# Optimization experiments

Measured on AMD Instinct MI355X. Metric: run time of the kernel, lower is better.

Reference implementation:

```python
import jax, jax.numpy as jnp
import numpy as np

TAU = 20.0   # membrane time constant (init default)
TH = 1.0     # spike threshold (init default)
K = 10.0     # surrogate sigmoid slope (hard-coded in forward)
EPS = 1e-6


def setup_inputs() -> dict:
    key = jax.random.key(0)
    I = jax.random.normal(key, (4096, 4096), dtype=jnp.float32)  # [B, L]
    return {"I": I}


def reference(I):
    B, L = I.shape

    def step(v, I_t):
        # Euler: dv = -v/tau + I ; v <- v + dv
        v = v - v / TAU + I_t
        s_soft = jax.nn.sigmoid(K * (v - TH))
        s_hard = (v >= TH).astype(I.dtype)
        # straight-through: value = s_hard, gradient flows through s_soft
        s = jax.lax.stop_gradient(s_hard - s_soft) + s_soft
        # reset: v <- v * (1 - stopgrad(s)); stopgrad(s) has value s_hard
        v = v * (1.0 - s_hard)
        return v, (s, s_hard)

    v0 = jnp.zeros((B,), dtype=I.dtype)
    _, (spikes_t, hard_t) = jax.lax.scan(step, v0, I.T)  # xs: [L, B]
    spikes = spikes_t.T       # [B, L]
    hard_spikes = hard_t.T    # [B, L]

    # hard latency: index of first hard spike, else L
    fired = hard_spikes > 0.5
    has = jnp.any(fired, axis=1)
    idx = jnp.argmax(fired, axis=1)
    hard_latency = jnp.where(has, idx, L).astype(jnp.int32)  # [B]

    # soft latency: spike-weighted mean time
    time = jnp.arange(L, dtype=spikes.dtype)
    w = spikes / (spikes.sum(axis=1, keepdims=True) + EPS)
    soft_latency = (w * time).sum(axis=1)  # [B]

    return spikes, hard_latency, soft_latency
```

## Files before the change

kernel.cpp:

```cpp
#include <hip/hip_runtime.h>

#define B_DIM 4096
#define L_DIM 4096
#define SEGLEN 512
#define NSEG (L_DIM / SEGLEN)
#define WARM 512
#define CHUNK 64
#define LSTRIDE 68

typedef float f4 __attribute__((ext_vector_type(4)));

__global__ __launch_bounds__(256) void init_kernel(float* wsf, int* wsi) {
    int i = blockIdx.x * 256 + threadIdx.x;
    if (i < 2 * B_DIM) wsf[i] = 0.f;
    if (i < B_DIM) wsi[i] = L_DIM;
}

#define LIF_CORE(IIN)                         \
    float q0 = u * cdiv;                      \
    float rr = fmaf(-20.0f, q0, u);           \
    float q  = fmaf(rr, cdiv, q0);            \
    float a  = u - q;                         \
    float b  = a + (IIN);                     \
    u = sp ? (IIN) : b;                       \
    sp = (u >= 1.0f);

#define WARM_STEP(IIN) { LIF_CORE(IIN) }

#define FULL_STEP(IIN, SOUT)                  \
    {                                         \
        LIF_CORE(IIN)                         \
        float sf = sp ? 1.0f : 0.0f;          \
        cnt += sf;                            \
        seen = fmaxf(seen, sf);               \
        accS += cnt;                          \
        accF += seen;                         \
        (SOUT) = sf;                          \
    }

__global__ __launch_bounds__(128, 1) void lif_kernel(const float* __restrict__ I,
                                                     float* __restrict__ out,
                                                     float* __restrict__ Cacc,
                                                     float* __restrict__ tsAcc,
                                                     int* __restrict__ firstAcc) {
    __shared__ __align__(16) float lds[2][64 * LSTRIDE];
    const int wid = threadIdx.x >> 6;
    const int lane = threadIdx.x & 63;
    const int seg = blockIdx.x >> 6;
    const int rowBase = (blockIdx.x & 63) * 64;
    const int t0 = seg * SEGLEN;
    const int start = (seg == 0) ? 0 : (t0 - WARM);
    const int nwarmCh = (seg == 0) ? 0 : (WARM / CHUNK);
    const int nch = nwarmCh + SEGLEN / CHUNK;

#define PROD_BAR() asm volatile("s_waitcnt lgkmcnt(0)\n\ts_barrier" ::: "memory")
#define COMP_BAR() asm volatile("s_barrier" ::: "memory")

    if (wid == 1) {
        const int srow = lane >> 4, scol = lane & 15;
        const float* gb = I + (size_t)rowBase * L_DIM + start + scol * 4;
        {
            float* dst = &lds[0][0];
#pragma unroll
            for (int p = 0; p < 16; ++p) {
                const int r = 4 * p + srow;
                f4 v = *(const f4*)(gb + (size_t)r * L_DIM);
                *(f4*)&dst[r * LSTRIDE + scol * 4] = v;
            }
        }
        PROD_BAR();
        for (int c = 0; c < nch; ++c) {
            if (c + 1 < nch) {
                const float* g = gb + (c + 1) * CHUNK;
                float* dst = &lds[(c + 1) & 1][0];
#pragma unroll
                for (int p = 0; p < 16; ++p) {
                    const int r = 4 * p + srow;
                    f4 v = *(const f4*)(g + (size_t)r * L_DIM);
                    *(f4*)&dst[r * LSTRIDE + scol * 4] = v;
                }
            }
            PROD_BAR();
        }
    } else {
        const int row = rowBase + lane;
        float u = 0.f, cnt = 0.f, seen = 0.f, accS = 0.f, accF = 0.f;
        bool sp = false;
        const float cdiv = 0.05f;
        float* so = out + (size_t)row * L_DIM + t0;

        COMP_BAR();
        for (int c = 0; c < nch; ++c) {
            const float* buf = &lds[c & 1][lane * LSTRIDE];
            f4 r0 = *(const f4*)(buf + 0),  r1 = *(const f4*)(buf + 4);
            f4 r2 = *(const f4*)(buf + 8),  r3 = *(const f4*)(buf + 12);
            f4 r4 = *(const f4*)(buf + 16), r5 = *(const f4*)(buf + 20);
            f4 r6 = *(const f4*)(buf + 24), r7 = *(const f4*)(buf + 28);
            f4 r8 = *(const f4*)(buf + 32), r9 = *(const f4*)(buf + 36);
            f4 r10 = *(const f4*)(buf + 40), r11 = *(const f4*)(buf + 44);
            f4 r12 = *(const f4*)(buf + 48), r13 = *(const f4*)(buf + 52);
            f4 r14 = *(const f4*)(buf + 56), r15 = *(const f4*)(buf + 60);
            asm volatile("" : "+v"(r0), "+v"(r1), "+v"(r2), "+v"(r3),
                             "+v"(r4), "+v"(r5), "+v"(r6), "+v"(r7),
                             "+v"(r8), "+v"(r9), "+v"(r10), "+v"(r11),
                             "+v"(r12), "+v"(r13), "+v"(r14), "+v"(r15));

            if (c < nwarmCh) {
#define WQ(RK) { WARM_STEP(RK.x) WARM_STEP(RK.y) WARM_STEP(RK.z) WARM_STEP(RK.w) }
                WQ(r0) WQ(r1) WQ(r2) WQ(r3) WQ(r4) WQ(r5) WQ(r6) WQ(r7)
                WQ(r8) WQ(r9) WQ(r10) WQ(r11) WQ(r12) WQ(r13) WQ(r14) WQ(r15)
#undef WQ
            } else {
                float* sd = so + (c - nwarmCh) * CHUNK;
#define FQ(RK, QI)                                                    \
                {                                                     \
                    f4 sv;                                            \
                    FULL_STEP(RK.x, sv.x) FULL_STEP(RK.y, sv.y)       \
                    FULL_STEP(RK.z, sv.z) FULL_STEP(RK.w, sv.w)       \
                    *(f4*)(sd + 4 * (QI)) = sv;                       \
                }
                FQ(r0, 0) FQ(r1, 1) FQ(r2, 2) FQ(r3, 3)
                FQ(r4, 4) FQ(r5, 5) FQ(r6, 6) FQ(r7, 7)
                FQ(r8, 8) FQ(r9, 9) FQ(r10, 10) FQ(r11, 11)
                FQ(r12, 12) FQ(r13, 13) FQ(r14, 14) FQ(r15, 15)
#undef FQ
            }
            COMP_BAR();
        }

        if (cnt > 0.f) {
            const int firstLocal = (int)((float)SEGLEN - accF);
            atomicMin(&firstAcc[row], t0 + firstLocal);
        }
        atomicAdd(&Cacc[row], cnt);
        atomicAdd(&tsAcc[row], fmaf((float)(t0 + SEGLEN), cnt, -accS));
    }
#undef PROD_BAR
#undef COMP_BAR
}

__global__ __launch_bounds__(256) void fin_kernel(const float* __restrict__ Cacc,
                                                  const float* __restrict__ tsAcc,
                                                  const int* __restrict__ firstAcc,
                                                  float* __restrict__ out) {
    int r = blockIdx.x * 256 + threadIdx.x;
    if (r < B_DIM) {
        out[(size_t)B_DIM * L_DIM + r] = (float)firstAcc[r];
        out[(size_t)B_DIM * L_DIM + B_DIM + r] = tsAcc[r] / (Cacc[r] + 1e-6f);
    }
}

extern "C" void kernel_launch(void* const* d_in, const int* in_sizes, int n_in,
                              void* d_out, int out_size, void* d_ws, size_t ws_size,
                              hipStream_t stream) {
    const float* I = (const float*)d_in[0];
    float* out = (float*)d_out;
    float* wsf = (float*)d_ws;
    int* wsi = (int*)((float*)d_ws + 2 * B_DIM);
    (void)in_sizes; (void)n_in; (void)out_size; (void)ws_size;

    init_kernel<<<(2 * B_DIM + 255) / 256, 256, 0, stream>>>(wsf, wsi);
    lif_kernel<<<NSEG * 64, 128, 0, stream>>>(I, out, wsf, wsf + B_DIM, wsi);
    fin_kernel<<<(B_DIM + 255) / 256, 256, 0, stream>>>(wsf, wsf + B_DIM, wsi, out);
}
```

Measured before the change: 135.8 us.

## Interleave two independent rows per lane and halve segment and chunk length

Each compute lane now advances two independent rows, interleaved step by step, so the serial LIF dependency chains can hide each other's latency. The reset select becomes a multiply by a mask inside an FMA. Segments shrink to 256 steps and chunks to 32, with 128 rows per block. The warm-up stays at 512 steps, so the redundant warm-up work grows relative to the useful segment length.

```diff
diff --git a/kernel.cpp b/kernel.cpp
--- a/kernel.cpp
+++ b/kernel.cpp
@@ -2,11 +2,13 @@
 
 #define B_DIM 4096
 #define L_DIM 4096
-#define SEGLEN 512
+#define SEGLEN 256
 #define NSEG (L_DIM / SEGLEN)
 #define WARM 512
-#define CHUNK 64
-#define LSTRIDE 68
+#define CHUNK 32
+#define CF4 (CHUNK / 4)
+#define LSTRIDE 36
+#define RPB 128
 
 typedef float f4 __attribute__((ext_vector_type(4)));
 
@@ -16,25 +18,29 @@
     if (i < B_DIM) wsi[i] = L_DIM;
 }
 
-#define LIF_CORE(IIN)                         \
-    float q0 = u * cdiv;                      \
-    float rr = fmaf(-20.0f, q0, u);           \
+#define LIF_CORE(U, SP, M, IIN)               \
+    float q0 = (U) * cdiv;                    \
+    float rr = fmaf(-20.0f, q0, (U));         \
     float q  = fmaf(rr, cdiv, q0);            \
-    float a  = u - q;                         \
-    float b  = a + (IIN);                     \
-    u = sp ? (IIN) : b;                       \
-    sp = (u >= 1.0f);
+    float a  = (U) - q;                       \
+    (U) = fmaf(a, (M), (IIN));                \
+    (SP) = ((U) >= 1.0f);
 
-#define WARM_STEP(IIN) { LIF_CORE(IIN) }
+#define WARM_STEP(U, SP, M, IIN)              \
+    {                                         \
+        LIF_CORE(U, SP, M, IIN)               \
+        (M) = (SP) ? 0.0f : 1.0f;             \
+    }
 
-#define FULL_STEP(IIN, SOUT)                  \
+#define FULL_STEP(U, SP, M, CNT, SEEN, AS, AF, IIN, SOUT) \
     {                                         \
-        LIF_CORE(IIN)                         \
-        float sf = sp ? 1.0f : 0.0f;          \
-        cnt += sf;                            \
-        seen = fmaxf(seen, sf);               \
-        accS += cnt;                          \
-        accF += seen;                         \
+        LIF_CORE(U, SP, M, IIN)               \
+        float sf = (SP) ? 1.0f : 0.0f;        \
+        (M) = 1.0f - sf;                      \
+        (CNT) += sf;                          \
+        (SEEN) = fmaxf((SEEN), sf);           \
+        (AS) += (CNT);                        \
+        (AF) += (SEEN);                       \
         (SOUT) = sf;                          \
     }
 
@@ -43,28 +49,29 @@
                                                      float* __restrict__ Cacc,
                                                      float* __restrict__ tsAcc,
                                                      int* __restrict__ firstAcc) {
-    __shared__ __align__(16) float lds[2][64 * LSTRIDE];
+    __shared__ __align__(16) float lds[2][RPB * LSTRIDE];
     const int wid = threadIdx.x >> 6;
     const int lane = threadIdx.x & 63;
-    const int seg = blockIdx.x >> 6;
-    const int rowBase = (blockIdx.x & 63) * 64;
+    const int seg = blockIdx.x >> 5;
+    const int rowBase = (blockIdx.x & 31) * RPB;
     const int t0 = seg * SEGLEN;
-    const int start = (seg == 0) ? 0 : (t0 - WARM);
-    const int nwarmCh = (seg == 0) ? 0 : (WARM / CHUNK);
+    const int start = (t0 > WARM) ? (t0 - WARM) : 0;
+    const int warmSteps = t0 - start;
+    const int nwarmCh = warmSteps / CHUNK;
     const int nch = nwarmCh + SEGLEN / CHUNK;
 
 #define PROD_BAR() asm volatile("s_waitcnt lgkmcnt(0)\n\ts_barrier" ::: "memory")
 #define COMP_BAR() asm volatile("s_barrier" ::: "memory")
 
     if (wid == 1) {
-        const int srow = lane >> 4, scol = lane & 15;
-        const float* gb = I + (size_t)rowBase * L_DIM + start + scol * 4;
+        const int srow = lane >> 3, scol = lane & 7;
+        const float* gb = I + (size_t)(rowBase + srow) * L_DIM + start + scol * 4;
         {
             float* dst = &lds[0][0];
 #pragma unroll
             for (int p = 0; p < 16; ++p) {
-                const int r = 4 * p + srow;
-                f4 v = *(const f4*)(gb + (size_t)r * L_DIM);
+                const int r = p * 8 + srow;
+                f4 v = *(const f4*)(gb + (size_t)(p * 8) * L_DIM);
                 *(f4*)&dst[r * LSTRIDE + scol * 4] = v;
             }
         }
@@ -75,65 +82,78 @@
                 float* dst = &lds[(c + 1) & 1][0];
 #pragma unroll
                 for (int p = 0; p < 16; ++p) {
-                    const int r = 4 * p + srow;
-                    f4 v = *(const f4*)(g + (size_t)r * L_DIM);
+                    const int r = p * 8 + srow;
+                    f4 v = *(const f4*)(g + (size_t)(p * 8) * L_DIM);
                     *(f4*)&dst[r * LSTRIDE + scol * 4] = v;
                 }
             }
             PROD_BAR();
         }
     } else {
-        const int row = rowBase + lane;
-        float u = 0.f, cnt = 0.f, seen = 0.f, accS = 0.f, accF = 0.f;
-        bool sp = false;
+        const int rowA = rowBase + lane, rowB = rowA + 64;
+        float uA = 0.f, cntA = 0.f, seenA = 0.f, asA = 0.f, afA = 0.f, mA = 1.f;
+        float uB = 0.f, cntB = 0.f, seenB = 0.f, asB = 0.f, afB = 0.f, mB = 1.f;
+        bool spA = false, spB = false;
         const float cdiv = 0.05f;
-        float* so = out + (size_t)row * L_DIM + t0;
+        float* soA = out + (size_t)rowA * L_DIM + t0;
+        float* soB = out + (size_t)rowB * L_DIM + t0;
 
         COMP_BAR();
         for (int c = 0; c < nch; ++c) {
-            const float* buf = &lds[c & 1][lane * LSTRIDE];
-            f4 r0 = *(const f4*)(buf + 0),  r1 = *(const f4*)(buf + 4);
-            f4 r2 = *(const f4*)(buf + 8),  r3 = *(const f4*)(buf + 12);
-            f4 r4 = *(const f4*)(buf + 16), r5 = *(const f4*)(buf + 20);
-            f4 r6 = *(const f4*)(buf + 24), r7 = *(const f4*)(buf + 28);
-            f4 r8 = *(const f4*)(buf + 32), r9 = *(const f4*)(buf + 36);
-            f4 r10 = *(const f4*)(buf + 40), r11 = *(const f4*)(buf + 44);
-            f4 r12 = *(const f4*)(buf + 48), r13 = *(const f4*)(buf + 52);
-            f4 r14 = *(const f4*)(buf + 56), r15 = *(const f4*)(buf + 60);
-            asm volatile("" : "+v"(r0), "+v"(r1), "+v"(r2), "+v"(r3),
-                             "+v"(r4), "+v"(r5), "+v"(r6), "+v"(r7),
-                             "+v"(r8), "+v"(r9), "+v"(r10), "+v"(r11),
-                             "+v"(r12), "+v"(r13), "+v"(r14), "+v"(r15));
+            const float* bufA = &lds[c & 1][lane * LSTRIDE];
+            const float* bufB = bufA + 64 * LSTRIDE;
+            f4 a0 = *(const f4*)(bufA + 0),  a1 = *(const f4*)(bufA + 4);
+            f4 a2 = *(const f4*)(bufA + 8),  a3 = *(const f4*)(bufA + 12);
+            f4 a4 = *(const f4*)(bufA + 16), a5 = *(const f4*)(bufA + 20);
+            f4 a6 = *(const f4*)(bufA + 24), a7 = *(const f4*)(bufA + 28);
+            f4 b0 = *(const f4*)(bufB + 0),  b1 = *(const f4*)(bufB + 4);
+            f4 b2 = *(const f4*)(bufB + 8),  b3 = *(const f4*)(bufB + 12);
+            f4 b4 = *(const f4*)(bufB + 16), b5 = *(const f4*)(bufB + 20);
+            f4 b6 = *(const f4*)(bufB + 24), b7 = *(const f4*)(bufB + 28);
+            asm volatile("" : "+v"(a0), "+v"(a1), "+v"(a2), "+v"(a3),
+                             "+v"(a4), "+v"(a5), "+v"(a6), "+v"(a7),
+                             "+v"(b0), "+v"(b1), "+v"(b2), "+v"(b3),
+                             "+v"(b4), "+v"(b5), "+v"(b6), "+v"(b7));
 
             if (c < nwarmCh) {
-#define WQ(RK) { WARM_STEP(RK.x) WARM_STEP(RK.y) WARM_STEP(RK.z) WARM_STEP(RK.w) }
-                WQ(r0) WQ(r1) WQ(r2) WQ(r3) WQ(r4) WQ(r5) WQ(r6) WQ(r7)
-                WQ(r8) WQ(r9) WQ(r10) WQ(r11) WQ(r12) WQ(r13) WQ(r14) WQ(r15)
+#define WQ(RA, RB)                                                     \
+                { WARM_STEP(uA, spA, mA, RA.x) WARM_STEP(uB, spB, mB, RB.x)  \
+                  WARM_STEP(uA, spA, mA, RA.y) WARM_STEP(uB, spB, mB, RB.y)  \
+                  WARM_STEP(uA, spA, mA, RA.z) WARM_STEP(uB, spB, mB, RB.z)  \
+                  WARM_STEP(uA, spA, mA, RA.w) WARM_STEP(uB, spB, mB, RB.w) }
+                WQ(a0, b0) WQ(a1, b1) WQ(a2, b2) WQ(a3, b3)
+                WQ(a4, b4) WQ(a5, b5) WQ(a6, b6) WQ(a7, b7)
 #undef WQ
             } else {
-                float* sd = so + (c - nwarmCh) * CHUNK;
-#define FQ(RK, QI)                                                    \
-                {                                                     \
-                    f4 sv;                                            \
-                    FULL_STEP(RK.x, sv.x) FULL_STEP(RK.y, sv.y)       \
-                    FULL_STEP(RK.z, sv.z) FULL_STEP(RK.w, sv.w)       \
-                    *(f4*)(sd + 4 * (QI)) = sv;                       \
+                float* sdA = soA + (c - nwarmCh) * CHUNK;
+                float* sdB = soB + (c - nwarmCh) * CHUNK;
+#define FS_A(IIN, SOUT) FULL_STEP(uA, spA, mA, cntA, seenA, asA, afA, IIN, SOUT)
+#define FS_B(IIN, SOUT) FULL_STEP(uB, spB, mB, cntB, seenB, asB, afB, IIN, SOUT)
+#define FQ(RA, RB, J)                                                  \
+                {                                                      \
+                    f4 svA, svB;                                       \
+                    FS_A(RA.x, svA.x) FS_B(RB.x, svB.x)                \
+                    FS_A(RA.y, svA.y) FS_B(RB.y, svB.y)                \
+                    FS_A(RA.z, svA.z) FS_B(RB.z, svB.z)                \
+                    FS_A(RA.w, svA.w) FS_B(RB.w, svB.w)                \
+                    *(f4*)(sdA + 4 * (J)) = svA;                       \
+                    *(f4*)(sdB + 4 * (J)) = svB;                       \
                 }
-                FQ(r0, 0) FQ(r1, 1) FQ(r2, 2) FQ(r3, 3)
-                FQ(r4, 4) FQ(r5, 5) FQ(r6, 6) FQ(r7, 7)
-                FQ(r8, 8) FQ(r9, 9) FQ(r10, 10) FQ(r11, 11)
-                FQ(r12, 12) FQ(r13, 13) FQ(r14, 14) FQ(r15, 15)
+                FQ(a0, b0, 0) FQ(a1, b1, 1) FQ(a2, b2, 2) FQ(a3, b3, 3)
+                FQ(a4, b4, 4) FQ(a5, b5, 5) FQ(a6, b6, 6) FQ(a7, b7, 7)
 #undef FQ
+#undef FS_A
+#undef FS_B
             }
             COMP_BAR();
         }
 
-        if (cnt > 0.f) {
-            const int firstLocal = (int)((float)SEGLEN - accF);
-            atomicMin(&firstAcc[row], t0 + firstLocal);
-        }
-        atomicAdd(&Cacc[row], cnt);
-        atomicAdd(&tsAcc[row], fmaf((float)(t0 + SEGLEN), cnt, -accS));
+        if (cntA > 0.f) atomicMin(&firstAcc[rowA], t0 + (int)((float)SEGLEN - afA));
+        atomicAdd(&Cacc[rowA], cntA);
+        atomicAdd(&tsAcc[rowA], fmaf((float)(t0 + SEGLEN), cntA, -asA));
+        if (cntB > 0.f) atomicMin(&firstAcc[rowB], t0 + (int)((float)SEGLEN - afB));
+        atomicAdd(&Cacc[rowB], cntB);
+        atomicAdd(&tsAcc[rowB], fmaf((float)(t0 + SEGLEN), cntB, -asB));
     }
 #undef PROD_BAR
 #undef COMP_BAR
@@ -160,6 +180,6 @@
     (void)in_sizes; (void)n_in; (void)out_size; (void)ws_size;
 
     init_kernel<<<(2 * B_DIM + 255) / 256, 256, 0, stream>>>(wsf, wsi);
-    lif_kernel<<<NSEG * 64, 128, 0, stream>>>(I, out, wsf, wsf + B_DIM, wsi);
+    lif_kernel<<<(B_DIM / RPB) * NSEG, 128, 0, stream>>>(I, out, wsf, wsf + B_DIM, wsi);
     fin_kernel<<<(B_DIM + 255) / 256, 256, 0, stream>>>(wsf, wsf + B_DIM, wsi, out);
 }
```

Result: slower. 143.7 us (+5.8%).
